# Performance work log

Measured on AMD Instinct MI355X. Metric: run time of the kernel, lower is better.

The kernel has to match this reference:

```python
import jax, jax.numpy as jnp
import numpy as np

# J2 (von Mises) plane-strain elastoplasticity with linear isotropic hardening
# (faithful stand-in for pyprnn's J2Material: elastic predictor + radial return,
#  committed history = plastic strain tensor + accumulated plastic strain).
E_MOD = 3130.0   # Young's modulus (epoxy, MPa)
NU = 0.37        # Poisson ratio
SIG_Y = 64.8     # initial yield stress
H_ISO = 300.0    # linear isotropic hardening modulus
MU = E_MOD / (2.0 * (1.0 + NU))
LAM = E_MOD * NU / ((1.0 + NU) * (1.0 - 2.0 * NU))


def j2_update(eps, eps_p, alpha):
    """eps: [P,3] (exx, eyy, gamma_xy engineering); eps_p: [P,4] (xx,yy,zz,xy tensorial);
    alpha: [P] accumulated plastic strain. Returns (stress [P,3], eps_p_new, alpha_new)."""
    ee_xx = eps[:, 0] - eps_p[:, 0]
    ee_yy = eps[:, 1] - eps_p[:, 1]
    ee_zz = -eps_p[:, 2]                      # plane strain: total ezz = 0
    ee_xy = 0.5 * eps[:, 2] - eps_p[:, 3]     # tensorial shear
    tr = ee_xx + ee_yy + ee_zz
    # trial (elastic predictor) stress
    sxx = LAM * tr + 2.0 * MU * ee_xx
    syy = LAM * tr + 2.0 * MU * ee_yy
    szz = LAM * tr + 2.0 * MU * ee_zz
    sxy = 2.0 * MU * ee_xy
    p = (sxx + syy + szz) / 3.0
    dxx, dyy, dzz = sxx - p, syy - p, szz - p
    q = jnp.sqrt(1.5 * (dxx * dxx + dyy * dyy + dzz * dzz + 2.0 * sxy * sxy))
    f = q - (SIG_Y + H_ISO * alpha)
    dgam = jnp.maximum(f, 0.0) / (3.0 * MU + H_ISO)   # radial return, closed form
    qs = jnp.maximum(q, 1e-12)
    nxx, nyy, nzz, nxy = 1.5 * dxx / qs, 1.5 * dyy / qs, 1.5 * dzz / qs, 1.5 * sxy / qs
    two_mu_dg = 2.0 * MU * dgam
    sig = jnp.stack([sxx - two_mu_dg * nxx, syy - two_mu_dg * nyy, sxy - two_mu_dg * nxy], axis=-1)
    eps_p_new = eps_p + dgam[:, None] * jnp.stack([nxx, nyy, nzz, nxy], axis=-1)
    alpha_new = alpha + dgam
    return sig, eps_p_new, alpha_new


def setup_inputs() -> dict:
    key = jax.random.key(0)
    k1, k2, k3 = jax.random.split(key, 3)
    B, T, F = 16384, 128, 3
    MATPTS = 16
    L, O = MATPTS * F, 3
    x = jax.random.normal(k1, (B, T, F), dtype=jnp.float32) * 0.02  # strain paths
    W1 = jax.random.normal(k2, (L, F), dtype=jnp.float32) * (1.0 / np.sqrt(F))
    W2 = jax.random.normal(k3, (O, L), dtype=jnp.float32) * (1.0 / np.sqrt(L))
    return {"x": x, "W1": W1, "W2": W2}


def reference(x, W1, W2):
    B, T, F = x.shape
    L = W1.shape[0]
    P = B * (L // F)                 # total material points = batch * mat_pts
    W2s = jax.nn.softplus(W2)        # SoftLayer: positive weights, no bias
    xt = jnp.swapaxes(x, 0, 1)       # [T, B, F]

    def step(carry, xi):
        eps_p, alpha = carry
        lat = xi @ W1.T                       # fc1 (no bias): [B, L]
        eps = lat.reshape(P, F)               # per-material-point strain
        sig, eps_p, alpha = j2_update(eps, eps_p, alpha)   # update + commit
        out = sig.reshape(B, L) @ W2s.T       # fc2 softplus-weighted linear
        return (eps_p, alpha), out

    carry0 = (jnp.zeros((P, 4), jnp.float32), jnp.zeros((P,), jnp.float32))
    _, ys = jax.lax.scan(step, carry0, xt)    # ys: [T, B, O]
    return jnp.swapaxes(ys, 0, 1)             # [B, T, O]
```

## Files before the change

kernel.cpp:

```cpp
#include <hip/hip_runtime.h>
#include <math.h>


#define BLOCK 256
#define BPB 32
#define TSTEPS 128
#define ROWF (TSTEPS * 3)
#define ROWP 388

typedef float v2 __attribute__((ext_vector_type(2)));

static __device__ __forceinline__ v2 vfma(v2 a, v2 b, v2 c) {
    return __builtin_elementwise_fma(a, b, c);
}
static __device__ __forceinline__ v2 vmax(v2 a, v2 b) {
    return __builtin_elementwise_max(a, b);
}

#define DPP_ST(r, ctrl) "v_add_f32_dpp %" #r ", %" #r ", %" #r " " ctrl \
                        " row_mask:0xf bank_mask:0xf\n\t"
#define DPP_STAGE(ctrl) \
    DPP_ST(0, ctrl) DPP_ST(1, ctrl) DPP_ST(2, ctrl)  DPP_ST(3, ctrl) \
    DPP_ST(4, ctrl) DPP_ST(5, ctrl) DPP_ST(6, ctrl)  DPP_ST(7, ctrl) \
    DPP_ST(8, ctrl) DPP_ST(9, ctrl) DPP_ST(10, ctrl) DPP_ST(11, ctrl)
#define DPP_BFLY12(a0,a1,a2,a3,a4,a5,a6,a7,a8,a9,a10,a11)                    \
  asm volatile(                                                              \
    "s_nop 1\n\t"                                                            \
    DPP_STAGE("quad_perm:[1,0,3,2]")                                         \
    DPP_STAGE("quad_perm:[2,3,0,1]")                                         \
    DPP_STAGE("row_half_mirror")                                             \
    : "+v"(a0), "+v"(a1), "+v"(a2), "+v"(a3), "+v"(a4), "+v"(a5),            \
      "+v"(a6), "+v"(a7), "+v"(a8), "+v"(a9), "+v"(a10), "+v"(a11))

__global__ __launch_bounds__(BLOCK, 2)
void prnn_j2_kernel(const float* __restrict__ x,
                    const float* __restrict__ W1,
                    const float* __restrict__ W2,
                    float* __restrict__ out)
{
    constexpr float MU    = (float)(3130.0 / (2.0 * (1.0 + 0.37)));
    constexpr float LAM   = (float)(3130.0 * 0.37 / ((1.0 + 0.37) * (1.0 - 2.0 * 0.37)));
    constexpr float SIG_Y = 64.8f;
    constexpr float H_ISO = 300.0f;
    const float TWO_MU  = 2.0f * MU;
    const float INV_DEN = 1.0f / (3.0f * MU + H_ISO);
    const float K3P     = (3.0f * MU) * INV_DEN;
    const float HP      = H_ISO * INV_DEN;
    const float KBULK   = LAM + TWO_MU * (1.0f / 3.0f);
    const float C_Q2    = 6.0f * MU * MU;

    __shared__ float xs[BPB * ROWP + 12];

    const int tid = threadIdx.x;
    const int g   = tid >> 3;
    const int l   = tid & 7;
    const int blockBase = blockIdx.x * (BPB * ROWF);

    {
        const float4* xg = (const float4*)(x + blockBase);
        for (int i4 = tid; i4 < BPB * ROWF / 4; i4 += BLOCK) {
            int b  = i4 / (ROWF / 4);
            int r4 = i4 - b * (ROWF / 4);
            ((float4*)(xs + b * ROWP))[r4] = xg[i4];
        }
    }

    const int pa = l, pb = l + 8;
    v2 w1p[3][3], w2p[3][3];
    #pragma unroll
    for (int c = 0; c < 3; ++c)
        #pragma unroll
        for (int f = 0; f < 3; ++f) {
            w1p[c][f].x = W1[(3 * pa + c) * 3 + f];
            w1p[c][f].y = W1[(3 * pb + c) * 3 + f];
        }
    #pragma unroll
    for (int o = 0; o < 3; ++o)
        #pragma unroll
        for (int c = 0; c < 3; ++c) {
            float wa = W2[o * 48 + 3 * pa + c];
            float wb = W2[o * 48 + 3 * pb + c];
            w2p[o][c].x = fmaxf(wa, 0.0f) + log1pf(expf(-fabsf(wa)));
            w2p[o][c].y = fmaxf(wb, 0.0f) + log1pf(expf(-fabsf(wb)));
        }

    __syncthreads();

    v2 p0 = {0.f,0.f}, p1 = {0.f,0.f}, p2 = {0.f,0.f}, p3 = {0.f,0.f};
    v2 yld = {SIG_Y, SIG_Y};
    float* xrow = &xs[g * ROWP];
    const float4* xv = (const float4*)xrow;
    const bool wact = (l < 3);

#define J2_PHYS(x0_, x1_, x2_, o0_, o1_, o2_)                                \
  {                                                                          \
    const float x0s = (x0_), x1s = (x1_), x2s = (x2_);                       \
    const v2 x0 = {x0s, x0s}, x1 = {x1s, x1s}, x2 = {x2s, x2s};              \
    const v2 e0 = vfma(w1p[0][0], x0, vfma(w1p[0][1], x1, w1p[0][2] * x2));  \
    const v2 e1 = vfma(w1p[1][0], x0, vfma(w1p[1][1], x1, w1p[1][2] * x2));  \
    const v2 e2 = vfma(w1p[2][0], x0, vfma(w1p[2][1], x1, w1p[2][2] * x2));  \
    const v2 ee_xx = e0 - p0;                                                \
    const v2 ee_yy = e1 - p1;                                                \
    const v2 ee_xy = 0.5f * e2 - p3;                                         \
    const v2 tr = (ee_xx + ee_yy) - p2;                                      \
    const v2 c3 = tr * (1.0f / 3.0f);                                        \
    const v2 exd = ee_xx - c3;                                               \
    const v2 eyd = ee_yy - c3;                                               \
    const v2 ezd = -p2 - c3;                                                 \
    v2 u = exd * exd;                                                        \
    u = vfma(eyd, eyd, u);                                                   \
    u = vfma(ezd, ezd, u);                                                   \
    u = vfma(ee_xy * ee_xy, (v2){2.0f, 2.0f}, u);                            \
    const v2 q2 = vmax(C_Q2 * u, (v2){1e-24f, 1e-24f});                      \
    v2 rq;                                                                   \
    rq.x = __builtin_amdgcn_rsqf(q2.x);                                      \
    rq.y = __builtin_amdgcn_rsqf(q2.y);                                      \
    const v2 q = q2 * rq;                                                    \
    const v2 f = vmax(q - yld, (v2){0.0f, 0.0f});                            \
    yld = vfma((v2){HP, HP}, f, yld);                                        \
    const v2 k   = (K3P * f) * rq;                                           \
    const v2 omk = 1.0f - k;                                                 \
    const v2 pm  = KBULK * tr;                                               \
    const v2 s0 = vfma(TWO_MU * exd, omk, pm);                               \
    const v2 s1 = vfma(TWO_MU * eyd, omk, pm);                               \
    const v2 s2 = (TWO_MU * ee_xy) * omk;                                    \
    p0 = vfma(k, exd, p0);                                                   \
    p1 = vfma(k, eyd, p1);                                                   \
    p2 = vfma(k, ezd, p2);                                                   \
    p3 = vfma(k, ee_xy, p3);                                                 \
    v2 r0 = vfma(w2p[0][0], s0, vfma(w2p[0][1], s1, w2p[0][2] * s2));        \
    v2 r1 = vfma(w2p[1][0], s0, vfma(w2p[1][1], s1, w2p[1][2] * s2));        \
    v2 r2 = vfma(w2p[2][0], s0, vfma(w2p[2][1], s1, w2p[2][2] * s2));        \
    o0_ = r0.x + r0.y;                                                       \
    o1_ = r1.x + r1.y;                                                       \
    o2_ = r2.x + r2.y;                                                       \
  }

    float4 A0 = xv[0], A1 = xv[1], A2 = xv[2];
    for (int tb = 0; tb < TSTEPS / 4; ++tb) {
        float4 An0 = xv[3 * tb + 3];
        float4 An1 = xv[3 * tb + 4];
        float4 An2 = xv[3 * tb + 5];

        float o00, o01, o02, o10, o11, o12, o20, o21, o22, o30, o31, o32;
        J2_PHYS(A0.x, A0.y, A0.z, o00, o01, o02);
        J2_PHYS(A0.w, A1.x, A1.y, o10, o11, o12);
        J2_PHYS(A1.z, A1.w, A2.x, o20, o21, o22);
        J2_PHYS(A2.y, A2.z, A2.w, o30, o31, o32);

        DPP_BFLY12(o00, o01, o02, o10, o11, o12,
                   o20, o21, o22, o30, o31, o32);

        if (wact) {
            float* wp = xrow + 12 * tb + l;
            float v0 = (l == 1) ? o01 : o00;  v0 = (l == 2) ? o02 : v0;
            float v1 = (l == 1) ? o11 : o10;  v1 = (l == 2) ? o12 : v1;
            float v2s = (l == 1) ? o21 : o20; v2s = (l == 2) ? o22 : v2s;
            float v3 = (l == 1) ? o31 : o30;  v3 = (l == 2) ? o32 : v3;
            wp[0] = v0;  wp[3] = v1;  wp[6] = v2s;  wp[9] = v3;
        }

        A0 = An0; A1 = An1; A2 = An2;
    }
#undef J2_PHYS

    __syncthreads();

    {
        float4* og = (float4*)(out + blockBase);
        for (int i4 = tid; i4 < BPB * ROWF / 4; i4 += BLOCK) {
            int b  = i4 / (ROWF / 4);
            int r4 = i4 - b * (ROWF / 4);
            og[i4] = ((const float4*)(xs + b * ROWP))[r4];
        }
    }
}

extern "C" void kernel_launch(void* const* d_in, const int* in_sizes, int n_in,
                              void* d_out, int out_size, void* d_ws, size_t ws_size,
                              hipStream_t stream) {
    const float* x  = (const float*)d_in[0];
    const float* W1 = (const float*)d_in[1];
    const float* W2 = (const float*)d_in[2];
    float* out = (float*)d_out;

    const int B = 16384;
    dim3 grid(B / BPB);
    dim3 block(BLOCK);
    prnn_j2_kernel<<<grid, block, 0, stream>>>(x, W1, W2, out);
}
```

Before: 120.5 us.

## Precompute linear stress response, accumulate plastic correction, drop LDS staging

```diff
diff --git a/kernel.cpp b/kernel.cpp
--- a/kernel.cpp
+++ b/kernel.cpp
@@ -6,7 +6,6 @@
 #define BPB 32
 #define TSTEPS 128
 #define ROWF (TSTEPS * 3)
-#define ROWP 388
 
 typedef float v2 __attribute__((ext_vector_type(2)));
 
@@ -16,6 +15,12 @@
 static __device__ __forceinline__ v2 vmax(v2 a, v2 b) {
     return __builtin_elementwise_max(a, b);
 }
+
+#define DPP_ADDST(v, ctrl)                                                   \
+    v += __int_as_float(__builtin_amdgcn_update_dpp(                         \
+        0, __float_as_int(v), (ctrl), 0xf, 0xf, true))
+#define RED8(v)                                                              \
+    do { DPP_ADDST(v, 0xB1); DPP_ADDST(v, 0x4E); DPP_ADDST(v, 0x141); } while (0)
 
 #define DPP_ST(r, ctrl) "v_add_f32_dpp %" #r ", %" #r ", %" #r " " ctrl \
                         " row_mask:0xf bank_mask:0xf\n\t"
@@ -46,24 +51,16 @@
     const float INV_DEN = 1.0f / (3.0f * MU + H_ISO);
     const float K3P     = (3.0f * MU) * INV_DEN;
     const float HP      = H_ISO * INV_DEN;
-    const float KBULK   = LAM + TWO_MU * (1.0f / 3.0f);
-    const float C_Q2    = 6.0f * MU * MU;
-
-    __shared__ float xs[BPB * ROWP + 12];
+    const float CSC     = 1.0f / (MU * 2.4494897427831781f);
+    const float Y0      = SIG_Y * CSC;
 
     const int tid = threadIdx.x;
     const int g   = tid >> 3;
     const int l   = tid & 7;
-    const int blockBase = blockIdx.x * (BPB * ROWF);
-
-    {
-        const float4* xg = (const float4*)(x + blockBase);
-        for (int i4 = tid; i4 < BPB * ROWF / 4; i4 += BLOCK) {
-            int b  = i4 / (ROWF / 4);
-            int r4 = i4 - b * (ROWF / 4);
-            ((float4*)(xs + b * ROWP))[r4] = xg[i4];
-        }
-    }
+    const int gb  = blockIdx.x * BPB + g;
+
+    const float* xb = x + gb * ROWF;
+    float* ob = out + gb * ROWF;
 
     const int pa = l, pb = l + 8;
     v2 w1p[3][3], w2p[3][3];
@@ -71,8 +68,9 @@
     for (int c = 0; c < 3; ++c)
         #pragma unroll
         for (int f = 0; f < 3; ++f) {
-            w1p[c][f].x = W1[(3 * pa + c) * 3 + f];
-            w1p[c][f].y = W1[(3 * pb + c) * 3 + f];
+            float s = (c == 2) ? 0.5f : 1.0f;
+            w1p[c][f].x = s * W1[(3 * pa + c) * 3 + f];
+            w1p[c][f].y = s * W1[(3 * pb + c) * 3 + f];
         }
     #pragma unroll
     for (int o = 0; o < 3; ++o)
@@ -84,96 +82,112 @@
             w2p[o][c].y = fmaxf(wb, 0.0f) + log1pf(expf(-fabsf(wb)));
         }
 
-    __syncthreads();
+    float Mrow[3];
+    {
+        float Ms[3][3];
+        #pragma unroll
+        for (int f = 0; f < 3; ++f) {
+            v2 ax = (LAM + TWO_MU) * w1p[0][f] + LAM * w1p[1][f];
+            v2 ay = LAM * w1p[0][f] + (LAM + TWO_MU) * w1p[1][f];
+            v2 as = TWO_MU * w1p[2][f];
+            #pragma unroll
+            for (int o = 0; o < 3; ++o) {
+                v2 mp = vfma(w2p[o][0], ax, vfma(w2p[o][1], ay, w2p[o][2] * as));
+                float ms = mp.x + mp.y;
+                RED8(ms);
+                Ms[o][f] = ms;
+            }
+        }
+        #pragma unroll
+        for (int f = 0; f < 3; ++f) {
+            float v = (l == 0) ? Ms[0][f] : ((l == 1) ? Ms[1][f] : Ms[2][f]);
+            Mrow[f] = v;
+        }
+    }
 
     v2 p0 = {0.f,0.f}, p1 = {0.f,0.f}, p2 = {0.f,0.f}, p3 = {0.f,0.f};
-    v2 yld = {SIG_Y, SIG_Y};
-    float* xrow = &xs[g * ROWP];
-    const float4* xv = (const float4*)xrow;
+    v2 Y  = {Y0, Y0};
+    v2 z0 = {0.f,0.f}, z1 = {0.f,0.f}, z2 = {0.f,0.f};
+
+    const float4* xv = (const float4*)xb;
     const bool wact = (l < 3);
-
-#define J2_PHYS(x0_, x1_, x2_, o0_, o1_, o2_)                                \
+    float* obl = ob + l;
+
+#define J2_PHYS(x0_, x1_, x2_, rr, mxv)                                      \
   {                                                                          \
     const float x0s = (x0_), x1s = (x1_), x2s = (x2_);                       \
     const v2 x0 = {x0s, x0s}, x1 = {x1s, x1s}, x2 = {x2s, x2s};              \
-    const v2 e0 = vfma(w1p[0][0], x0, vfma(w1p[0][1], x1, w1p[0][2] * x2));  \
-    const v2 e1 = vfma(w1p[1][0], x0, vfma(w1p[1][1], x1, w1p[1][2] * x2));  \
-    const v2 e2 = vfma(w1p[2][0], x0, vfma(w1p[2][1], x1, w1p[2][2] * x2));  \
-    const v2 ee_xx = e0 - p0;                                                \
-    const v2 ee_yy = e1 - p1;                                                \
-    const v2 ee_xy = 0.5f * e2 - p3;                                         \
+    const v2 ee_xx = vfma(w1p[0][0], x0, vfma(w1p[0][1], x1,                 \
+                          vfma(w1p[0][2], x2, -p0)));                        \
+    const v2 ee_yy = vfma(w1p[1][0], x0, vfma(w1p[1][1], x1,                 \
+                          vfma(w1p[1][2], x2, -p1)));                        \
+    const v2 ee_xy = vfma(w1p[2][0], x0, vfma(w1p[2][1], x1,                 \
+                          vfma(w1p[2][2], x2, -p3)));                        \
     const v2 tr = (ee_xx + ee_yy) - p2;                                      \
     const v2 c3 = tr * (1.0f / 3.0f);                                        \
     const v2 exd = ee_xx - c3;                                               \
     const v2 eyd = ee_yy - c3;                                               \
-    const v2 ezd = -p2 - c3;                                                 \
+    const v2 szd = exd + eyd;                                    \
+    const v2 t2 = ee_xy * ee_xy;                                             \
     v2 u = exd * exd;                                                        \
     u = vfma(eyd, eyd, u);                                                   \
-    u = vfma(ezd, ezd, u);                                                   \
-    u = vfma(ee_xy * ee_xy, (v2){2.0f, 2.0f}, u);                            \
-    const v2 q2 = vmax(C_Q2 * u, (v2){1e-24f, 1e-24f});                      \
+    u = vfma(szd, szd, u);                                                   \
+    u = vfma(t2, (v2){2.0f, 2.0f}, u);                                       \
+    u = vmax(u, (v2){1e-30f, 1e-30f});                                       \
     v2 rq;                                                                   \
-    rq.x = __builtin_amdgcn_rsqf(q2.x);                                      \
-    rq.y = __builtin_amdgcn_rsqf(q2.y);                                      \
-    const v2 q = q2 * rq;                                                    \
-    const v2 f = vmax(q - yld, (v2){0.0f, 0.0f});                            \
-    yld = vfma((v2){HP, HP}, f, yld);                                        \
-    const v2 k   = (K3P * f) * rq;                                           \
-    const v2 omk = 1.0f - k;                                                 \
-    const v2 pm  = KBULK * tr;                                               \
-    const v2 s0 = vfma(TWO_MU * exd, omk, pm);                               \
-    const v2 s1 = vfma(TWO_MU * eyd, omk, pm);                               \
-    const v2 s2 = (TWO_MU * ee_xy) * omk;                                    \
-    p0 = vfma(k, exd, p0);                                                   \
-    p1 = vfma(k, eyd, p1);                                                   \
-    p2 = vfma(k, ezd, p2);                                                   \
-    p3 = vfma(k, ee_xy, p3);                                                 \
-    v2 r0 = vfma(w2p[0][0], s0, vfma(w2p[0][1], s1, w2p[0][2] * s2));        \
-    v2 r1 = vfma(w2p[1][0], s0, vfma(w2p[1][1], s1, w2p[1][2] * s2));        \
-    v2 r2 = vfma(w2p[2][0], s0, vfma(w2p[2][1], s1, w2p[2][2] * s2));        \
-    o0_ = r0.x + r0.y;                                                       \
-    o1_ = r1.x + r1.y;                                                       \
-    o2_ = r2.x + r2.y;                                                       \
+    rq.x = __builtin_amdgcn_rsqf(u.x);                                       \
+    rq.y = __builtin_amdgcn_rsqf(u.y);                                       \
+    const v2 su = u * rq;                                       \
+    const v2 fY = vmax(su - Y, (v2){0.0f, 0.0f});                            \
+    Y = vfma((v2){HP, HP}, fY, Y);                                           \
+    const v2 k = (K3P * fY) * rq;                                            \
+    const v2 kdx = k * exd;                                                  \
+    const v2 kdy = k * eyd;                                                  \
+    const v2 kdxy = k * ee_xy;                                               \
+    p0 += kdx;                                                               \
+    p1 += kdy;                                                               \
+    p3 += kdxy;                                                              \
+    p2 = p2 - k * szd;                                                       \
+    z0 = vfma(w2p[0][0], kdx, vfma(w2p[0][1], kdy, vfma(w2p[0][2], kdxy, z0)));\
+    z1 = vfma(w2p[1][0], kdx, vfma(w2p[1][1], kdy, vfma(w2p[1][2], kdxy, z1)));\
+    z2 = vfma(w2p[2][0], kdx, vfma(w2p[2][1], kdy, vfma(w2p[2][2], kdxy, z2)));\
+    (rr)[0] = z0.x + z0.y;                                                   \
+    (rr)[1] = z1.x + z1.y;                                                   \
+    (rr)[2] = z2.x + z2.y;                                                   \
+    (mxv) = fmaf(Mrow[0], x0s, fmaf(Mrow[1], x1s, Mrow[2] * x2s));           \
   }
 
     float4 A0 = xv[0], A1 = xv[1], A2 = xv[2];
+
     for (int tb = 0; tb < TSTEPS / 4; ++tb) {
-        float4 An0 = xv[3 * tb + 3];
-        float4 An1 = xv[3 * tb + 4];
-        float4 An2 = xv[3 * tb + 5];
-
-        float o00, o01, o02, o10, o11, o12, o20, o21, o22, o30, o31, o32;
-        J2_PHYS(A0.x, A0.y, A0.z, o00, o01, o02);
-        J2_PHYS(A0.w, A1.x, A1.y, o10, o11, o12);
-        J2_PHYS(A1.z, A1.w, A2.x, o20, o21, o22);
-        J2_PHYS(A2.y, A2.z, A2.w, o30, o31, o32);
-
-        DPP_BFLY12(o00, o01, o02, o10, o11, o12,
-                   o20, o21, o22, o30, o31, o32);
+        const int nb = (tb < TSTEPS / 4 - 1) ? (3 * tb + 3) : (3 * tb);
+        float4 An0 = xv[nb + 0];
+        float4 An1 = xv[nb + 1];
+        float4 An2 = xv[nb + 2];
+
+        float r[12], mx[4];
+        J2_PHYS(A0.x,  A0.y,  A0.z,  r + 0, mx[0]);
+        J2_PHYS(A0.w,  A1.x,  A1.y,  r + 3, mx[1]);
+        J2_PHYS(A1.z,  A1.w,  A2.x,  r + 6, mx[2]);
+        J2_PHYS(A2.y,  A2.z,  A2.w,  r + 9, mx[3]);
+
+        DPP_BFLY12(r[0], r[1], r[2], r[3], r[4], r[5],
+                   r[6], r[7], r[8], r[9], r[10], r[11]);
 
         if (wact) {
-            float* wp = xrow + 12 * tb + l;
-            float v0 = (l == 1) ? o01 : o00;  v0 = (l == 2) ? o02 : v0;
-            float v1 = (l == 1) ? o11 : o10;  v1 = (l == 2) ? o12 : v1;
-            float v2s = (l == 1) ? o21 : o20; v2s = (l == 2) ? o22 : v2s;
-            float v3 = (l == 1) ? o31 : o30;  v3 = (l == 2) ? o32 : v3;
-            wp[0] = v0;  wp[3] = v1;  wp[6] = v2s;  wp[9] = v3;
+            float zz0 = (l == 0) ? r[0] : ((l == 1) ? r[1]  : r[2]);
+            float zz1 = (l == 0) ? r[3] : ((l == 1) ? r[4]  : r[5]);
+            float zz2 = (l == 0) ? r[6] : ((l == 1) ? r[7]  : r[8]);
+            float zz3 = (l == 0) ? r[9] : ((l == 1) ? r[10] : r[11]);
+            obl[12 * tb + 0] = fmaf(-TWO_MU, zz0, mx[0]);
+            obl[12 * tb + 3] = fmaf(-TWO_MU, zz1, mx[1]);
+            obl[12 * tb + 6] = fmaf(-TWO_MU, zz2, mx[2]);
+            obl[12 * tb + 9] = fmaf(-TWO_MU, zz3, mx[3]);
         }
 
         A0 = An0; A1 = An1; A2 = An2;
     }
 #undef J2_PHYS
-
-    __syncthreads();
-
-    {
-        float4* og = (float4*)(out + blockBase);
-        for (int i4 = tid; i4 < BPB * ROWF / 4; i4 += BLOCK) {
-            int b  = i4 / (ROWF / 4);
-            int r4 = i4 - b * (ROWF / 4);
-            og[i4] = ((const float4*)(xs + b * ROWP))[r4];
-        }
-    }
 }
 
 extern "C" void kernel_launch(void* const* d_in, const int* in_sizes, int n_in,
```

Measured after the change: 116.7 us. -3.1%, faster.
